# Optimization experiments

Measured on AMD Instinct MI355X. Metric: run time of the kernel, lower is better.

Reference implementation:

```python
import jax, jax.numpy as jnp
import numpy as np

MOMENTUM = 0.01  # scalar momentum, init kwarg; trainable=False, initialization='unbiased', causal=True


def _ema_scan(x, m):
    """y[t] = (1-m)*y[t-1] + m*x[t], y[-1]=0, via log-depth associative scan over last axis."""
    a = jnp.full_like(x, 1.0 - m)
    b = m * x

    def combine(c1, c2):
        a1, b1 = c1
        a2, b2 = c2
        return a1 * a2, a2 * b1 + b2

    _, y = jax.lax.associative_scan(combine, (a, b), axis=-1)
    return y


def _bias_correction(num_samples, m, dtype):
    # correction[t] = 1 / (1 - (1-m)^(t+1)), t = 0..T-1
    power = jnp.arange(1, 1 + num_samples, dtype=dtype)
    return 1.0 / (1.0 - jnp.power(jnp.asarray(1.0 - m, dtype=dtype), power))


def setup_inputs() -> dict:
    key = jax.random.key(0)
    x = jax.random.normal(key, (32, 256, 8192), dtype=jnp.float32)
    return {"x": x}


def reference(x) -> jnp.ndarray:
    T = x.shape[-1]
    y = _ema_scan(x, MOMENTUM)
    corr = _bias_correction(T, MOMENTUM, x.dtype)  # [T], broadcasts over leading dims
    return y * corr
```

## Files before the change

### kernel.cpp

```cpp
#include <hip/hip_runtime.h>


namespace {

constexpr int T = 8192;
constexpr int BLOCK = 256;
constexpr int CHUNK = T / BLOCK;
constexpr int NWAVE = BLOCK / 64;
constexpr int VECS = T / (4 * BLOCK);

__device__ __forceinline__ int sw(int p) { return p ^ ((p >> 5) & 31); }

__global__ __launch_bounds__(BLOCK) void ema_kernel(const float* __restrict__ x,
                                                    float* __restrict__ out) {
  __shared__ float sm[T];
  __shared__ float smW[NWAVE];

  const int tid = threadIdx.x;
  const long long base = (long long)blockIdx.x * (long long)T;

  const float4* xv = reinterpret_cast<const float4*>(x + base);
#pragma unroll
  for (int k = 0; k < VECS; ++k) {
    const int u = tid + BLOCK * k;
    const float4 v = xv[u];
    const int p = 4 * u;
    sm[sw(p + 0)] = v.x;
    sm[sw(p + 1)] = v.y;
    sm[sw(p + 2)] = v.z;
    sm[sw(p + 3)] = v.w;
  }
  __syncthreads();

  constexpr float A1 = 0.99f, M = 0.01f;
  constexpr float A2 = A1 * A1;
  constexpr float A4 = A2 * A2;
  constexpr float A8 = A4 * A4;
  constexpr float A16 = A8 * A8;
  constexpr float A32 = A16 * A16;
  constexpr float A64 = A32 * A32;
  constexpr float A128 = A64 * A64;
  constexpr float A256 = A128 * A128;
  constexpr float A512 = A256 * A256;
  constexpr float A1024 = A512 * A512;
  constexpr float A2048 = A1024 * A1024;
  constexpr float A4096 = A2048 * A2048;

  const int cbase = tid * CHUNK;
  float acc[CHUNK];
  float run = 0.0f;
#pragma unroll
  for (int e = 0; e < CHUNK; ++e) {
    run = fmaf(run, A1, M * sm[sw(cbase + e)]);
    acc[e] = run;
  }

  const int lane = tid & 63;
  const int w = tid >> 6;

  float S = run;
  {
    float t;
    t = __shfl_up(S, 1, 64);  if (lane >= 1)  S = fmaf(t, A32,   S);
    t = __shfl_up(S, 2, 64);  if (lane >= 2)  S = fmaf(t, A64,   S);
    t = __shfl_up(S, 4, 64);  if (lane >= 4)  S = fmaf(t, A128,  S);
    t = __shfl_up(S, 8, 64);  if (lane >= 8)  S = fmaf(t, A256,  S);
    t = __shfl_up(S, 16, 64); if (lane >= 16) S = fmaf(t, A512,  S);
    t = __shfl_up(S, 32, 64); if (lane >= 32) S = fmaf(t, A1024, S);
  }
  if (lane == 63) smW[w] = S;
  const float Sprev = __shfl_up(S, 1, 64);
  __syncthreads();

  float Q = 0.0f;
#pragma unroll
  for (int v = 0; v < NWAVE - 1; ++v) {
    if (v < w) Q = fmaf(Q, A2048, smW[v]);
  }

  float Dlane = 1.0f;
  if (lane & 1)  Dlane *= A32;
  if (lane & 2)  Dlane *= A64;
  if (lane & 4)  Dlane *= A128;
  if (lane & 8)  Dlane *= A256;
  if (lane & 16) Dlane *= A512;
  if (lane & 32) Dlane *= A1024;

  const float carry = (lane ? Sprev : 0.0f) + Dlane * Q;

  float Pt = 1.0f;
  if (tid & 1)   Pt *= A32;
  if (tid & 2)   Pt *= A64;
  if (tid & 4)   Pt *= A128;
  if (tid & 8)   Pt *= A256;
  if (tid & 16)  Pt *= A512;
  if (tid & 32)  Pt *= A1024;
  if (tid & 64)  Pt *= A2048;
  if (tid & 128) Pt *= A4096;

  float pw = 1.0f;
#pragma unroll
  for (int e = 0; e < CHUNK; ++e) {
    pw *= A1;
    Pt *= A1;
    const float yv = fmaf(carry, pw, acc[e]);
    const float corr = __builtin_amdgcn_rcpf(1.0f - Pt);
    sm[sw(cbase + e)] = yv * corr;
  }
  __syncthreads();

  float4* ov = reinterpret_cast<float4*>(out + base);
#pragma unroll
  for (int k = 0; k < VECS; ++k) {
    const int u = tid + BLOCK * k;
    const int p = 4 * u;
    float4 v;
    v.x = sm[sw(p + 0)];
    v.y = sm[sw(p + 1)];
    v.z = sm[sw(p + 2)];
    v.w = sm[sw(p + 3)];
    ov[u] = v;
  }
}

}

extern "C" void kernel_launch(void* const* d_in, const int* in_sizes, int n_in,
                              void* d_out, int out_size, void* d_ws, size_t ws_size,
                              hipStream_t stream) {
  const float* x = (const float*)d_in[0];
  float* out = (float*)d_out;
  const int rows = in_sizes[0] / T;
  ema_kernel<<<dim3(rows), dim3(BLOCK), 0, stream>>>(x, out);
}
```

Before: 429.6 us.

## Load rows straight into LDS, write outputs from registers, skip saturated bias correction

Input rows are now loaded with global_load_lds directly into a float4-swizzled shared buffer, and each thread reads its chunk back as float4 vectors instead of doing scalar swizzled stores and loads. Outputs are written straight from registers as float4 per thread, which removes the second shared-memory round trip and its barrier. Only the first wave applies the bias-correction reciprocal, since for later positions the factor rounds to 1.0 in fp32. Launch bounds now request higher occupancy. The trade-off is that each thread writes its own contiguous 128-byte span, so a single store instruction is spread across many cache lines rather than coalesced across lanes.

New measurement: 441.6 us. 1.03x slower.

```diff
diff --git a/kernel.cpp b/kernel.cpp
--- a/kernel.cpp
+++ b/kernel.cpp
@@ -7,29 +7,28 @@
 constexpr int BLOCK = 256;
 constexpr int CHUNK = T / BLOCK;
 constexpr int NWAVE = BLOCK / 64;
-constexpr int VECS = T / (4 * BLOCK);
+constexpr int V4 = T / 4;
+constexpr int VPT = V4 / BLOCK;
 
-__device__ __forceinline__ int sw(int p) { return p ^ ((p >> 5) & 31); }
+__device__ __forceinline__ int sw4(int v) { return v ^ ((v >> 3) & 7); }
 
-__global__ __launch_bounds__(BLOCK) void ema_kernel(const float* __restrict__ x,
-                                                    float* __restrict__ out) {
-  __shared__ float sm[T];
-  __shared__ float smW[NWAVE];
+__global__ __launch_bounds__(BLOCK, 5) void ema_kernel(const float* __restrict__ x,
+                                                       float* __restrict__ out) {
+  __shared__ float4 sm4[V4];
 
   const int tid = threadIdx.x;
   const long long base = (long long)blockIdx.x * (long long)T;
 
   const float4* xv = reinterpret_cast<const float4*>(x + base);
 #pragma unroll
-  for (int k = 0; k < VECS; ++k) {
-    const int u = tid + BLOCK * k;
-    const float4 v = xv[u];
-    const int p = 4 * u;
-    sm[sw(p + 0)] = v.x;
-    sm[sw(p + 1)] = v.y;
-    sm[sw(p + 2)] = v.z;
-    sm[sw(p + 3)] = v.w;
+  for (int k = 0; k < VPT; ++k) {
+    const int slot = tid + BLOCK * k;
+    const int g = sw4(slot);
+    __builtin_amdgcn_global_load_lds(
+        (const __attribute__((address_space(1))) void*)(xv + g),
+        (__attribute__((address_space(3))) void*)(sm4 + slot), 16, 0, 0);
   }
+  asm volatile("s_waitcnt vmcnt(0)" ::: "memory");
   __syncthreads();
 
   constexpr float A1 = 0.99f, M = 0.01f;
@@ -44,15 +43,17 @@
   constexpr float A512 = A256 * A256;
   constexpr float A1024 = A512 * A512;
   constexpr float A2048 = A1024 * A1024;
-  constexpr float A4096 = A2048 * A2048;
 
-  const int cbase = tid * CHUNK;
+  const int vbase = tid * VPT;
   float acc[CHUNK];
   float run = 0.0f;
 #pragma unroll
-  for (int e = 0; e < CHUNK; ++e) {
-    run = fmaf(run, A1, M * sm[sw(cbase + e)]);
-    acc[e] = run;
+  for (int e4 = 0; e4 < VPT; ++e4) {
+    const float4 v = sm4[sw4(vbase + e4)];
+    run = fmaf(run, A1, M * v.x); acc[4 * e4 + 0] = run;
+    run = fmaf(run, A1, M * v.y); acc[4 * e4 + 1] = run;
+    run = fmaf(run, A1, M * v.z); acc[4 * e4 + 2] = run;
+    run = fmaf(run, A1, M * v.w); acc[4 * e4 + 3] = run;
   }
 
   const int lane = tid & 63;
@@ -68,8 +69,11 @@
     t = __shfl_up(S, 16, 64); if (lane >= 16) S = fmaf(t, A512,  S);
     t = __shfl_up(S, 32, 64); if (lane >= 32) S = fmaf(t, A1024, S);
   }
+  const float Sprev = __shfl_up(S, 1, 64);
+
+  __syncthreads();
+  float* smW = reinterpret_cast<float*>(sm4);
   if (lane == 63) smW[w] = S;
-  const float Sprev = __shfl_up(S, 1, 64);
   __syncthreads();
 
   float Q = 0.0f;
@@ -88,38 +92,40 @@
 
   const float carry = (lane ? Sprev : 0.0f) + Dlane * Q;
 
-  float Pt = 1.0f;
-  if (tid & 1)   Pt *= A32;
-  if (tid & 2)   Pt *= A64;
-  if (tid & 4)   Pt *= A128;
-  if (tid & 8)   Pt *= A256;
-  if (tid & 16)  Pt *= A512;
-  if (tid & 32)  Pt *= A1024;
-  if (tid & 64)  Pt *= A2048;
-  if (tid & 128) Pt *= A4096;
+  float4* ov = reinterpret_cast<float4*>(out + base);
+  float pw = 1.0f;
 
-  float pw = 1.0f;
+  if (w == 0) {
+    float Pt = 1.0f;
+    if (tid & 1)  Pt *= A32;
+    if (tid & 2)  Pt *= A64;
+    if (tid & 4)  Pt *= A128;
+    if (tid & 8)  Pt *= A256;
+    if (tid & 16) Pt *= A512;
+    if (tid & 32) Pt *= A1024;
 #pragma unroll
-  for (int e = 0; e < CHUNK; ++e) {
-    pw *= A1;
-    Pt *= A1;
-    const float yv = fmaf(carry, pw, acc[e]);
-    const float corr = __builtin_amdgcn_rcpf(1.0f - Pt);
-    sm[sw(cbase + e)] = yv * corr;
-  }
-  __syncthreads();
-
-  float4* ov = reinterpret_cast<float4*>(out + base);
+    for (int e4 = 0; e4 < VPT; ++e4) {
+      float4 o;
+      pw *= A1; Pt *= A1;
+      o.x = fmaf(carry, pw, acc[4 * e4 + 0]) * __builtin_amdgcn_rcpf(1.0f - Pt);
+      pw *= A1; Pt *= A1;
+      o.y = fmaf(carry, pw, acc[4 * e4 + 1]) * __builtin_amdgcn_rcpf(1.0f - Pt);
+      pw *= A1; Pt *= A1;
+      o.z = fmaf(carry, pw, acc[4 * e4 + 2]) * __builtin_amdgcn_rcpf(1.0f - Pt);
+      pw *= A1; Pt *= A1;
+      o.w = fmaf(carry, pw, acc[4 * e4 + 3]) * __builtin_amdgcn_rcpf(1.0f - Pt);
+      ov[vbase + e4] = o;
+    }
+  } else {
 #pragma unroll
-  for (int k = 0; k < VECS; ++k) {
-    const int u = tid + BLOCK * k;
-    const int p = 4 * u;
-    float4 v;
-    v.x = sm[sw(p + 0)];
-    v.y = sm[sw(p + 1)];
-    v.z = sm[sw(p + 2)];
-    v.w = sm[sw(p + 3)];
-    ov[u] = v;
+    for (int e4 = 0; e4 < VPT; ++e4) {
+      float4 o;
+      pw *= A1; o.x = fmaf(carry, pw, acc[4 * e4 + 0]);
+      pw *= A1; o.y = fmaf(carry, pw, acc[4 * e4 + 1]);
+      pw *= A1; o.z = fmaf(carry, pw, acc[4 * e4 + 2]);
+      pw *= A1; o.w = fmaf(carry, pw, acc[4 * e4 + 3]);
+      ov[vbase + e4] = o;
+    }
   }
 }
 
```
